# Kernel tuning notes

Measured on AMD Instinct MI355X. Metric: run time of the kernel, lower is better.

The kernel has to match this reference:

```python
import jax, jax.numpy as jnp
import numpy as np

N_HEADS = 12

def setup_inputs() -> dict:
    key = jax.random.key(0)
    k1, k2, k3 = jax.random.split(key, 3)
    B, N, D = 2, 2048, 768
    x = jax.random.normal(k1, (B, N, D), dtype=jnp.float32)
    # Linear weights stored as [in, out] (equivalent to torch W.T)
    Wkqv = jax.random.normal(k2, (D, 3 * D), dtype=jnp.float32) * (1.0 / np.sqrt(D))
    bkqv = jnp.zeros((3 * D,), dtype=jnp.float32)
    Wproj = jax.random.normal(k3, (D, D), dtype=jnp.float32) * (1.0 / np.sqrt(D))
    bproj = jnp.zeros((D,), dtype=jnp.float32)
    return {"x": x, "Wkqv": Wkqv, "bkqv": bkqv, "Wproj": Wproj, "bproj": bproj}


def reference(x, Wkqv, bkqv, Wproj, bproj):
    B, N, D = x.shape
    H = N_HEADS
    hd = D // H
    kqv = x @ Wkqv + bkqv                     # [B, N, 3D]
    # NOTE: original chunks in (k, q, v) order
    k, q, v = jnp.split(kqv, 3, axis=-1)
    k = k.reshape(B, N, H, hd).transpose(0, 2, 1, 3)   # [B, H, N, hd]
    q = q.reshape(B, N, H, hd).transpose(0, 2, 1, 3)
    v = v.reshape(B, N, H, hd).transpose(0, 2, 1, 3)
    att = jnp.einsum('bhqd,bhkd->bhqk', q, k) / jnp.sqrt(jnp.float32(hd))
    causal = jnp.tril(jnp.ones((N, N), dtype=bool))    # [N, N]
    att = jnp.where(causal[None, None, :, :], att, jnp.float32(-jnp.inf))
    w = jax.nn.softmax(att, axis=-1)
    sa = jnp.einsum('bhqk,bhkd->bhqd', w, v)           # [B, H, N, hd]
    sa = sa.transpose(0, 2, 1, 3).reshape(B, N, D)
    return sa @ Wproj + bproj
```

## Files before the change

### kernel.cpp

```cpp
#include <hip/hip_runtime.h>

typedef __attribute__((ext_vector_type(8))) short bf16x8;
typedef __attribute__((ext_vector_type(4))) float f32x4;
typedef __attribute__((ext_vector_type(16))) float f32x16;

#define BATCH 2
#define SEQ 2048
#define DMODEL 768
#define NH 12
#define HD 64
#define M_TOK (BATCH * SEQ)
#define N_KQV (3 * DMODEL)

#define GLOAD16(gsrc, ldst) __builtin_amdgcn_global_load_lds( \
    (const __attribute__((address_space(1))) unsigned int*)(const void*)(gsrc), \
    (__attribute__((address_space(3))) unsigned int*)(void*)(ldst), 16, 0, 0)

__device__ __forceinline__ unsigned short f2bf(float f) {
  unsigned int u = __float_as_uint(f);
  u += 0x7FFFu + ((u >> 16) & 1u);
  return (unsigned short)(u >> 16);
}

__device__ __forceinline__ unsigned int cvtpk(float lo, float hi) {
  unsigned int r;
  asm("v_cvt_pk_bf16_f32 %0, %1, %2" : "=v"(r) : "v"(lo), "v"(hi));
  return r;
}

#define NB_CVT 3072
#define NB_T1 (72 * 24)
#define NB_T2 (24 * 24)

__global__ __launch_bounds__(256) void prep_kernel(
    const float* __restrict__ x, unsigned short* __restrict__ x_bf,
    const float* __restrict__ Wkqv, unsigned short* __restrict__ wkqvT,
    const float* __restrict__ Wproj, unsigned short* __restrict__ wprojT) {
  const int b = blockIdx.x;
  if (b < NB_CVT) {
    int i = b * 256 + threadIdx.x;
    float4 v = reinterpret_cast<const float4*>(x)[i];
    unsigned long long p = (unsigned long long)f2bf(v.x)
                         | ((unsigned long long)f2bf(v.y) << 16)
                         | ((unsigned long long)f2bf(v.z) << 32)
                         | ((unsigned long long)f2bf(v.w) << 48);
    reinterpret_cast<unsigned long long*>(x_bf)[i] = p;
    return;
  }
  __shared__ float tile[32][33];
  const float* in;
  unsigned short* out;
  int rows, cols, bx, by;
  if (b < NB_CVT + NB_T1) {
    int j = b - NB_CVT;
    in = Wkqv; out = wkqvT; rows = DMODEL; cols = N_KQV;
    bx = j % 72; by = j / 72;
  } else {
    int j = b - NB_CVT - NB_T1;
    in = Wproj; out = wprojT; rows = DMODEL; cols = DMODEL;
    bx = j % 24; by = j / 24;
  }
  const int tx = threadIdx.x & 31, ty = threadIdx.x >> 5;
  int c0 = bx * 32, r0 = by * 32;
  for (int i = ty; i < 32; i += 8)
    tile[i][tx] = in[(size_t)(r0 + i) * cols + c0 + tx];
  __syncthreads();
  for (int i = ty; i < 32; i += 8)
    out[(size_t)(c0 + i) * rows + r0 + tx] = f2bf(tile[tx][i]);
}

template <int MODE>
__global__ __launch_bounds__(512) void gemm_8w(
    const unsigned short* __restrict__ A,
    const unsigned short* __restrict__ BT,
    const float* __restrict__ bias,
    int NTOT,
    unsigned short* __restrict__ outK, unsigned short* __restrict__ outQ,
    unsigned short* __restrict__ outVT, float* __restrict__ outF) {
  constexpr int K = DMODEL;
  __shared__ __align__(16) unsigned short lds_a[3][128][32];
  __shared__ __align__(16) unsigned short lds_b[3][128][32];
  const int tid = threadIdx.x;
  const int lane = tid & 63;
  const int w = tid >> 6;
  const int wr = (w & 3) * 32;
  const int wc = (w >> 2) * 64;
  const int l31 = lane & 31, hi = lane >> 5;
  const int m0 = blockIdx.y * 128, n0 = blockIdx.x * 128;

  f32x16 acc[2];
#pragma unroll
  for (int nj = 0; nj < 2; nj++)
#pragma unroll
    for (int i = 0; i < 16; i++) acc[nj][i] = 0.f;

  const int srow = lane >> 2;
  const int sg = ((lane & 3) ^ ((lane >> 3) & 3)) * 8;
  const int xq = (l31 >> 1) & 3;

#define STAGE(buf, k0)                                                         \
  {                                                                            \
    if (w < 4) {                                                               \
      GLOAD16(&A[(size_t)(m0 + w * 32 + srow) * K + (k0) + sg],                \
              &lds_a[buf][w * 32][0]);                                         \
      GLOAD16(&A[(size_t)(m0 + w * 32 + 16 + srow) * K + (k0) + sg],           \
              &lds_a[buf][w * 32 + 16][0]);                                    \
    } else {                                                                   \
      GLOAD16(&BT[(size_t)(n0 + (w - 4) * 32 + srow) * K + (k0) + sg],         \
              &lds_b[buf][(w - 4) * 32][0]);                                   \
      GLOAD16(&BT[(size_t)(n0 + (w - 4) * 32 + 16 + srow) * K + (k0) + sg],    \
              &lds_b[buf][(w - 4) * 32 + 16][0]);                              \
    }                                                                          \
  }

  const int KT = K >> 5;
  STAGE(0, 0);
  STAGE(1, 32);

  int cur = 0;
  for (int kt = 0; kt < KT; ++kt) {
    if (kt + 1 < KT) asm volatile("s_waitcnt vmcnt(2)" ::: "memory");
    else             asm volatile("s_waitcnt vmcnt(0)" ::: "memory");
    __builtin_amdgcn_s_barrier();
    __builtin_amdgcn_sched_barrier(0);

    bf16x8 aA[2], aB[2][2];
#pragma unroll
    for (int ds = 0; ds < 2; ds++) {
      const int rc = ((ds * 2 + hi) ^ xq) * 8;
      aA[ds] = *(const bf16x8*)&lds_a[cur][wr + l31][rc];
#pragma unroll
      for (int nj = 0; nj < 2; nj++)
        aB[ds][nj] = *(const bf16x8*)&lds_b[cur][wc + nj * 32 + l31][rc];
    }
#pragma unroll
    for (int ds = 0; ds < 2; ds++)
#pragma unroll
      for (int nj = 0; nj < 2; nj++)
        acc[nj] = __builtin_amdgcn_mfma_f32_32x32x16_bf16(aA[ds], aB[ds][nj], acc[nj], 0, 0, 0);

    if (kt + 2 < KT) {
      const int nb = (cur + 2 >= 3) ? cur - 1 : cur + 2;
      STAGE(nb, (kt + 2) << 5);
    }
    cur = (cur == 2) ? 0 : cur + 1;
  }
#undef STAGE

#pragma unroll
  for (int nj = 0; nj < 2; nj++) {
#pragma unroll
    for (int r = 0; r < 16; r++) {
      int row = m0 + wr + (r & 3) + 8 * (r >> 2) + 4 * hi;
      int col = n0 + wc + nj * 32 + l31;
      float v = acc[nj][r] + bias[col];
      if (MODE == 0) {
        int chunk = col / DMODEL;
        int d = col - chunk * DMODEL;
        int hh = d >> 6, di = d & 63;
        int bb = row >> 11, tok = row & 2047;
        int bh = bb * NH + hh;
        if (chunk == 0)
          outK[((size_t)bh * SEQ + tok) * HD + di] = f2bf(v);
        else if (chunk == 1)
          outQ[((size_t)bh * SEQ + tok) * HD + di] = f2bf(v * 0.125f);
        else
          outVT[((size_t)bh * HD + di) * SEQ + tok] = f2bf(v);
      } else {
        outF[(size_t)row * NTOT + col] = v;
      }
    }
  }
}

__global__ __launch_bounds__(128) void attn_kernel(
    const unsigned short* __restrict__ qbuf,
    const unsigned short* __restrict__ kbuf,
    const unsigned short* __restrict__ vT,
    unsigned short* __restrict__ sa) {
  __shared__ __align__(16) char smem_raw[18432];
  auto k_lds = reinterpret_cast<unsigned short (*)[72]>(smem_raw);
  auto v_lds = reinterpret_cast<unsigned short (*)[72]>(smem_raw + 9216);
  auto o_merge = reinterpret_cast<float (*)[32][33]>(smem_raw);
  auto l_merge = reinterpret_cast<float (*)[32]>(smem_raw + 9216);

  const int tid = threadIdx.x, lane = tid & 63, w = tid >> 6;
  const int l31 = lane & 31, hi = lane >> 5;

  const int fid = (int)blockIdx.y * (int)gridDim.x + (int)blockIdx.x;
  const int xcd = fid & 7, slot = fid >> 3;
  const int head3 = slot % 3;
  const int t = 63 - slot / 3;
  const int bh = head3 * 8 + xcd;
  const int ktmax = t >> 1;

  const size_t qk_base = (size_t)bh * SEQ * HD;
  const size_t v_base = (size_t)bh * HD * SEQ;
  const int bb = bh / NH, h = bh - bb * NH;

  const int sr = w * 32 + (lane >> 3);
  const int sc = (lane & 7) * 8;

  {
    bf16x8 rk[4], rv[4];
#pragma unroll
    for (int p = 0; p < 4; p++) {
      rk[p] = *(const bf16x8*)&kbuf[qk_base + (size_t)(sr + 8 * p) * HD + sc];
      rv[p] = *(const bf16x8*)&vT[v_base + (size_t)(sr + 8 * p) * SEQ + sc];
    }
#pragma unroll
    for (int p = 0; p < 4; p++) {
      *(bf16x8*)&k_lds[sr + 8 * p][sc] = rk[p];
      *(bf16x8*)&v_lds[sr + 8 * p][sc] = rv[p];
    }
  }

  bf16x8 aq[4];
#pragma unroll
  for (int ds = 0; ds < 4; ds++)
    aq[ds] = *(const bf16x8*)&qbuf[qk_base + (size_t)(t * 32 + l31) * HD + ds * 16 + hi * 8];

  f32x16 o0, o1;
#pragma unroll
  for (int i = 0; i < 16; i++) { o0[i] = 0.f; o1[i] = 0.f; }
  float lsum = 0.f;

  __syncthreads();

  for (int kt = 0; kt <= ktmax; ++kt) {
    const bool more = (kt < ktmax);
    bf16x8 rk[4], rv[4];
    if (more) {
      const int nrow = (kt + 1) * 64;
#pragma unroll
      for (int p = 0; p < 4; p++) {
        rk[p] = *(const bf16x8*)&kbuf[qk_base + (size_t)(nrow + sr + 8 * p) * HD + sc];
        rv[p] = *(const bf16x8*)&vT[v_base + (size_t)(sr + 8 * p) * SEQ + nrow + sc];
      }
    }

    f32x16 s;
#pragma unroll
    for (int i = 0; i < 16; i++) s[i] = 0.f;
    __builtin_amdgcn_s_setprio(1);
#pragma unroll
    for (int ds = 0; ds < 4; ds++) {
      bf16x8 bk = *(const bf16x8*)&k_lds[w * 32 + l31][ds * 16 + hi * 8];
      s = __builtin_amdgcn_mfma_f32_32x32x16_bf16(bk, aq[ds], s, 0, 0, 0);
    }
    __builtin_amdgcn_s_setprio(0);

    const bool diag = (kt == ktmax);
    const int qb2 = (t & 1) * 32;
#pragma unroll
    for (int r = 0; r < 16; r++) {
      int kr = (r & 3) + 8 * (r >> 2) + 4 * hi;
      float val = s[r];
      if (diag && (w * 32 + kr > qb2 + l31)) val = -1e30f;
      float p = __expf(val);
      s[r] = p;
      lsum += p;
    }

    union { unsigned int u[4]; bf16x8 v; } f1, f2;
    {
      unsigned int A = cvtpk(s[0], s[1]), B = cvtpk(s[2], s[3]);
      unsigned int C = cvtpk(s[4], s[5]), D = cvtpk(s[6], s[7]);
      auto rAC = __builtin_amdgcn_permlane32_swap(A, C, false, false);
      auto rBD = __builtin_amdgcn_permlane32_swap(B, D, false, false);
      f1.u[0] = rAC[0]; f1.u[1] = rBD[0]; f1.u[2] = rAC[1]; f1.u[3] = rBD[1];
      unsigned int A2 = cvtpk(s[8], s[9]),   B2 = cvtpk(s[10], s[11]);
      unsigned int C2 = cvtpk(s[12], s[13]), D2 = cvtpk(s[14], s[15]);
      auto rAC2 = __builtin_amdgcn_permlane32_swap(A2, C2, false, false);
      auto rBD2 = __builtin_amdgcn_permlane32_swap(B2, D2, false, false);
      f2.u[0] = rAC2[0]; f2.u[1] = rBD2[0]; f2.u[2] = rAC2[1]; f2.u[3] = rBD2[1];
    }

    __builtin_amdgcn_s_setprio(1);
    {
      bf16x8 bv00 = *(const bf16x8*)&v_lds[l31][w * 32 + hi * 8];
      bf16x8 bv01 = *(const bf16x8*)&v_lds[32 + l31][w * 32 + hi * 8];
      o0 = __builtin_amdgcn_mfma_f32_32x32x16_bf16(f1.v, bv00, o0, 0, 0, 0);
      o1 = __builtin_amdgcn_mfma_f32_32x32x16_bf16(f1.v, bv01, o1, 0, 0, 0);
      bf16x8 bv10 = *(const bf16x8*)&v_lds[l31][w * 32 + 16 + hi * 8];
      bf16x8 bv11 = *(const bf16x8*)&v_lds[32 + l31][w * 32 + 16 + hi * 8];
      o0 = __builtin_amdgcn_mfma_f32_32x32x16_bf16(f2.v, bv10, o0, 0, 0, 0);
      o1 = __builtin_amdgcn_mfma_f32_32x32x16_bf16(f2.v, bv11, o1, 0, 0, 0);
    }
    __builtin_amdgcn_s_setprio(0);

    if (more) {
      __syncthreads();
#pragma unroll
      for (int p = 0; p < 4; p++) {
        *(bf16x8*)&k_lds[sr + 8 * p][sc] = rk[p];
        *(bf16x8*)&v_lds[sr + 8 * p][sc] = rv[p];
      }
      __syncthreads();
    }
  }

  __syncthreads();
  {
    float ltot = lsum + __shfl_xor(lsum, 32);
    if (hi == 0) l_merge[w][l31] = ltot;
    f32x16 osend = w ? o0 : o1;
#pragma unroll
    for (int r = 0; r < 16; r++) {
      int ql = (r & 3) + 8 * (r >> 2) + 4 * hi;
      o_merge[w][ql][l31] = osend[r];
    }
    __syncthreads();
    f32x16 okeep = w ? o1 : o0;
#pragma unroll
    for (int r = 0; r < 16; r++) {
      int ql = (r & 3) + 8 * (r >> 2) + 4 * hi;
      float ot = okeep[r] + o_merge[1 - w][ql][l31];
      float lt = l_merge[0][ql] + l_merge[1][ql];
      sa[((size_t)bb * SEQ + t * 32 + ql) * DMODEL + h * HD + w * 32 + l31] = f2bf(ot / lt);
    }
  }
}


extern "C" void kernel_launch(void* const* d_in, const int* in_sizes, int n_in,
                              void* d_out, int out_size, void* d_ws, size_t ws_size,
                              hipStream_t stream) {
  const float* x     = (const float*)d_in[0];
  const float* Wkqv  = (const float*)d_in[1];
  const float* bkqv  = (const float*)d_in[2];
  const float* Wproj = (const float*)d_in[3];
  const float* bproj = (const float*)d_in[4];
  float* out = (float*)d_out;

  char* ws = (char*)d_ws;
  unsigned short* x_bf   = (unsigned short*)(ws + 0);
  unsigned short* wkqvT  = (unsigned short*)(ws + 6291456);
  unsigned short* wprojT = (unsigned short*)(ws + 9830400);
  unsigned short* qb     = (unsigned short*)(ws + 11010048);
  unsigned short* kb     = (unsigned short*)(ws + 17301504);
  unsigned short* vT     = (unsigned short*)(ws + 23592960);
  unsigned short* sa     = (unsigned short*)(ws + 29884416);

  prep_kernel<<<NB_CVT + NB_T1 + NB_T2, 256, 0, stream>>>(
      x, x_bf, Wkqv, wkqvT, Wproj, wprojT);

  gemm_8w<0><<<dim3(N_KQV / 128, M_TOK / 128), 512, 0, stream>>>(
      x_bf, wkqvT, bkqv, N_KQV, kb, qb, vT, nullptr);

  attn_kernel<<<dim3(64, BATCH * NH), 128, 0, stream>>>(qb, kb, vT, sa);

  gemm_8w<1><<<dim3(DMODEL / 128, M_TOK / 128), 512, 0, stream>>>(
      sa, wprojT, bproj, DMODEL, nullptr, nullptr, nullptr, out);
}
```

Measured before the change: 100.8 us.

## Replace 8-wave 128x128 GEMM with single-wave 64x64 tiles and XCD-aware block mapping

Both projection GEMMs now use one wavefront per block computing a 64x64 tile with a 2x2 grid of MFMA accumulators, double-buffered LDS and no block barriers. Blocks are remapped so consecutive row tiles land on the same XCD, aiming for better L2 reuse. The goal is more blocks for occupancy and no inter-wave synchronisation. The cost is lower data reuse per block and more global traffic per FLOP.

After: 99.73 us (median of 2 runs). No clear change (-1.1%).

```diff
diff --git a/kernel.cpp b/kernel.cpp
--- a/kernel.cpp
+++ b/kernel.cpp
@@ -1,7 +1,6 @@
 #include <hip/hip_runtime.h>
 
 typedef __attribute__((ext_vector_type(8))) short bf16x8;
-typedef __attribute__((ext_vector_type(4))) float f32x4;
 typedef __attribute__((ext_vector_type(16))) float f32x16;
 
 #define BATCH 2
@@ -69,8 +68,8 @@
     out[(size_t)(c0 + i) * rows + r0 + tx] = f2bf(tile[tx][i]);
 }
 
-template <int MODE>
-__global__ __launch_bounds__(512) void gemm_8w(
+template <int NBX, int MODE>
+__global__ __launch_bounds__(64) void gemm_wi(
     const unsigned short* __restrict__ A,
     const unsigned short* __restrict__ BT,
     const float* __restrict__ bias,
@@ -78,96 +77,103 @@
     unsigned short* __restrict__ outK, unsigned short* __restrict__ outQ,
     unsigned short* __restrict__ outVT, float* __restrict__ outF) {
   constexpr int K = DMODEL;
-  __shared__ __align__(16) unsigned short lds_a[3][128][32];
-  __shared__ __align__(16) unsigned short lds_b[3][128][32];
-  const int tid = threadIdx.x;
-  const int lane = tid & 63;
-  const int w = tid >> 6;
-  const int wr = (w & 3) * 32;
-  const int wc = (w >> 2) * 64;
+  __shared__ __align__(16) unsigned short lds_a[2][64][32];
+  __shared__ __align__(16) unsigned short lds_b[2][64][32];
+  const int lane = threadIdx.x & 63;
   const int l31 = lane & 31, hi = lane >> 5;
-  const int m0 = blockIdx.y * 128, n0 = blockIdx.x * 128;
-
-  f32x16 acc[2];
-#pragma unroll
-  for (int nj = 0; nj < 2; nj++)
-#pragma unroll
-    for (int i = 0; i < 16; i++) acc[nj][i] = 0.f;
+
+  const int fid = (int)blockIdx.x;
+  const int xcd = fid & 7, slot = fid >> 3;
+  const int by = xcd * 8 + (slot & 7);
+  const int bx = slot >> 3;
+  const int m0 = by * 64, n0 = bx * 64;
+
+  f32x16 acc[2][2];
+#pragma unroll
+  for (int mi = 0; mi < 2; mi++)
+#pragma unroll
+    for (int nj = 0; nj < 2; nj++)
+#pragma unroll
+      for (int i = 0; i < 16; i++) acc[mi][nj][i] = 0.f;
 
   const int srow = lane >> 2;
   const int sg = ((lane & 3) ^ ((lane >> 3) & 3)) * 8;
   const int xq = (l31 >> 1) & 3;
 
-#define STAGE(buf, k0)                                                         \
-  {                                                                            \
-    if (w < 4) {                                                               \
-      GLOAD16(&A[(size_t)(m0 + w * 32 + srow) * K + (k0) + sg],                \
-              &lds_a[buf][w * 32][0]);                                         \
-      GLOAD16(&A[(size_t)(m0 + w * 32 + 16 + srow) * K + (k0) + sg],           \
-              &lds_a[buf][w * 32 + 16][0]);                                    \
-    } else {                                                                   \
-      GLOAD16(&BT[(size_t)(n0 + (w - 4) * 32 + srow) * K + (k0) + sg],         \
-              &lds_b[buf][(w - 4) * 32][0]);                                   \
-      GLOAD16(&BT[(size_t)(n0 + (w - 4) * 32 + 16 + srow) * K + (k0) + sg],    \
-              &lds_b[buf][(w - 4) * 32 + 16][0]);                              \
-    }                                                                          \
+#define STAGE(buf, k0)                                                        \
+  {                                                                           \
+    _Pragma("unroll")                                                         \
+    for (int rr = 0; rr < 4; ++rr)                                            \
+      GLOAD16(&A[(size_t)(m0 + rr * 16 + srow) * K + (k0) + sg],              \
+              &lds_a[buf][rr * 16][0]);                                       \
+    _Pragma("unroll")                                                         \
+    for (int rr = 0; rr < 4; ++rr)                                            \
+      GLOAD16(&BT[(size_t)(n0 + rr * 16 + srow) * K + (k0) + sg],             \
+              &lds_b[buf][rr * 16][0]);                                       \
   }
 
   const int KT = K >> 5;
   STAGE(0, 0);
   STAGE(1, 32);
 
-  int cur = 0;
   for (int kt = 0; kt < KT; ++kt) {
-    if (kt + 1 < KT) asm volatile("s_waitcnt vmcnt(2)" ::: "memory");
+    const int cur = kt & 1;
+    if (kt + 1 < KT) asm volatile("s_waitcnt vmcnt(8)" ::: "memory");
     else             asm volatile("s_waitcnt vmcnt(0)" ::: "memory");
-    __builtin_amdgcn_s_barrier();
     __builtin_amdgcn_sched_barrier(0);
 
-    bf16x8 aA[2], aB[2][2];
+    bf16x8 aA[2][2], aB[2][2];
 #pragma unroll
     for (int ds = 0; ds < 2; ds++) {
       const int rc = ((ds * 2 + hi) ^ xq) * 8;
-      aA[ds] = *(const bf16x8*)&lds_a[cur][wr + l31][rc];
+#pragma unroll
+      for (int mi = 0; mi < 2; mi++)
+        aA[ds][mi] = *(const bf16x8*)&lds_a[cur][mi * 32 + l31][rc];
 #pragma unroll
       for (int nj = 0; nj < 2; nj++)
-        aB[ds][nj] = *(const bf16x8*)&lds_b[cur][wc + nj * 32 + l31][rc];
+        aB[ds][nj] = *(const bf16x8*)&lds_b[cur][nj * 32 + l31][rc];
     }
 #pragma unroll
     for (int ds = 0; ds < 2; ds++)
 #pragma unroll
-      for (int nj = 0; nj < 2; nj++)
-        acc[nj] = __builtin_amdgcn_mfma_f32_32x32x16_bf16(aA[ds], aB[ds][nj], acc[nj], 0, 0, 0);
+      for (int mi = 0; mi < 2; mi++)
+#pragma unroll
+        for (int nj = 0; nj < 2; nj++)
+          acc[mi][nj] = __builtin_amdgcn_mfma_f32_32x32x16_bf16(
+              aA[ds][mi], aB[ds][nj], acc[mi][nj], 0, 0, 0);
 
     if (kt + 2 < KT) {
-      const int nb = (cur + 2 >= 3) ? cur - 1 : cur + 2;
-      STAGE(nb, (kt + 2) << 5);
-    }
-    cur = (cur == 2) ? 0 : cur + 1;
+      asm volatile("s_waitcnt lgkmcnt(0)" ::: "memory");
+      __builtin_amdgcn_sched_barrier(0);
+      STAGE(cur, (kt + 2) << 5);
+    }
   }
 #undef STAGE
 
 #pragma unroll
-  for (int nj = 0; nj < 2; nj++) {
-#pragma unroll
-    for (int r = 0; r < 16; r++) {
-      int row = m0 + wr + (r & 3) + 8 * (r >> 2) + 4 * hi;
-      int col = n0 + wc + nj * 32 + l31;
-      float v = acc[nj][r] + bias[col];
-      if (MODE == 0) {
-        int chunk = col / DMODEL;
-        int d = col - chunk * DMODEL;
-        int hh = d >> 6, di = d & 63;
-        int bb = row >> 11, tok = row & 2047;
-        int bh = bb * NH + hh;
-        if (chunk == 0)
-          outK[((size_t)bh * SEQ + tok) * HD + di] = f2bf(v);
-        else if (chunk == 1)
-          outQ[((size_t)bh * SEQ + tok) * HD + di] = f2bf(v * 0.125f);
-        else
-          outVT[((size_t)bh * HD + di) * SEQ + tok] = f2bf(v);
-      } else {
-        outF[(size_t)row * NTOT + col] = v;
+  for (int mi = 0; mi < 2; mi++) {
+#pragma unroll
+    for (int nj = 0; nj < 2; nj++) {
+#pragma unroll
+      for (int r = 0; r < 16; r++) {
+        int row = m0 + mi * 32 + (r & 3) + 8 * (r >> 2) + 4 * hi;
+        int col = n0 + nj * 32 + l31;
+        float v = acc[mi][nj][r] + bias[col];
+        if (MODE == 0) {
+          int chunk = col / DMODEL;
+          int d = col - chunk * DMODEL;
+          int hh = d >> 6, di = d & 63;
+          int bb = row >> 11, tok = row & 2047;
+          int bh = bb * NH + hh;
+          if (chunk == 0)
+            outK[((size_t)bh * SEQ + tok) * HD + di] = f2bf(v);
+          else if (chunk == 1)
+            outQ[((size_t)bh * SEQ + tok) * HD + di] = f2bf(v * 0.125f);
+          else
+            outVT[((size_t)bh * HD + di) * SEQ + tok] = f2bf(v);
+        } else {
+          outF[(size_t)row * NTOT + col] = v;
+        }
       }
     }
   }
@@ -345,11 +351,11 @@
   prep_kernel<<<NB_CVT + NB_T1 + NB_T2, 256, 0, stream>>>(
       x, x_bf, Wkqv, wkqvT, Wproj, wprojT);
 
-  gemm_8w<0><<<dim3(N_KQV / 128, M_TOK / 128), 512, 0, stream>>>(
+  gemm_wi<N_KQV / 64, 0><<<2304, 64, 0, stream>>>(
       x_bf, wkqvT, bkqv, N_KQV, kb, qb, vT, nullptr);
 
   attn_kernel<<<dim3(64, BATCH * NH), 128, 0, stream>>>(qb, kb, vT, sa);
 
-  gemm_8w<1><<<dim3(DMODEL / 128, M_TOK / 128), 512, 0, stream>>>(
+  gemm_wi<DMODEL / 64, 1><<<768, 64, 0, stream>>>(
       sa, wprojT, bproj, DMODEL, nullptr, nullptr, nullptr, out);
 }
```
